# Kernel tuning notes

Hardware: AMD Instinct MI355X
Metric: run time of the kernel (lower is better)

The kernel has to match this reference:

```python
import jax, jax.numpy as jnp
import numpy as np

B, N, H, D, L = 2, 256, 256, 64, 6  # batch, pocket atoms, hidden dim, atom feat dim, EGNN layers


def _lin(x, w, b):
    return x @ w + b


def setup_inputs() -> dict:
    key = jax.random.key(0)
    ks = iter(jax.random.split(key, 64))

    def w(shape, s=0.05):
        return jax.random.normal(next(ks), shape, jnp.float32) * s

    inp = {
        'pocket_coords': jax.random.normal(next(ks), (B, N, 3), jnp.float32),
        'pocket_features': jax.random.normal(next(ks), (B, N, D), jnp.float32),
        't': jax.random.uniform(next(ks), (B,), jnp.float32, 0.0, 1000.0),
        'pe_w1': w((3 + D, H)), 'pe_b1': w((H,)),
        'pe_w2': w((H, H)), 'pe_b2': w((H,)),
        'pe_w3': w((H, H)), 'pe_b3': w((H,)),
        'te_w1': w((1, H)), 'te_b1': w((H,)),
        'te_w2': w((H, H)), 'te_b2': w((H,)),
        'ln_g': jnp.ones((L, H), jnp.float32), 'ln_b': jnp.zeros((L, H), jnp.float32),
        'ew1': w((L, 2 * H + 1, H)), 'eb1': w((L, H)),
        'ew2': w((L, H, H)), 'eb2': w((L, H)),
        'cw1': w((L, H, H)), 'cb1': w((L, H)),
        'cw2': w((L, H, 1)), 'cb2': w((L, 1)),
        'nw1': w((L, 2 * H, H)), 'nb1': w((L, H)),
        'nw2': w((L, H, H)), 'nb2': w((L, H)),
        'dec_w1': w((H, H)), 'dec_b1': w((H,)),
        'dec_w2': w((H, H)), 'dec_b2': w((H,)),
        'dec_w3': w((H, 3)), 'dec_b3': w((3,)),
    }
    return inp


def reference(pocket_coords, pocket_features, t,
              pe_w1, pe_b1, pe_w2, pe_b2, pe_w3, pe_b3,
              te_w1, te_b1, te_w2, te_b2,
              ln_g, ln_b,
              ew1, eb1, ew2, eb2,
              cw1, cb1, cw2, cb2,
              nw1, nb1, nw2, nb2,
              dec_w1, dec_b1, dec_w2, dec_b2, dec_w3, dec_b3):
    relu, silu = jax.nn.relu, jax.nn.silu

    # --- pocket encoder (residual MLP; in_dim 67 != H so no skip; dropout = identity at eval)
    pin = jnp.concatenate([pocket_coords, pocket_features], axis=-1)  # [B,N,3+D]
    h = relu(_lin(pin, pe_w1, pe_b1))
    h = relu(_lin(h, pe_w2, pe_b2))
    h = relu(_lin(h, pe_w3, pe_b3))

    # --- time embedding, broadcast over atoms
    te = relu(_lin(t[:, None], te_w1, te_b1))
    te = _lin(te, te_w2, te_b2)  # [B,H]
    h = h + te[:, None, :]

    # --- 6-layer dense EGNN (all-pairs), norm_feats=True -> LayerNorm on h per layer
    x = pocket_coords
    for l in range(L):
        h_in = h
        mu = h.mean(-1, keepdims=True)
        hc = h - mu
        hn = hc / jnp.sqrt((hc * hc).mean(-1, keepdims=True) + 1e-5) * ln_g[l] + ln_b[l]
        rel = x[:, :, None, :] - x[:, None, :, :]            # [B,N,N,3]
        d2 = jnp.sum(rel * rel, axis=-1, keepdims=True)      # [B,N,N,1]
        hi = jnp.broadcast_to(hn[:, :, None, :], (B, N, N, H))
        hj = jnp.broadcast_to(hn[:, None, :, :], (B, N, N, H))
        eij = jnp.concatenate([hi, hj, d2], axis=-1)         # [B,N,N,2H+1]
        m = silu(_lin(eij, ew1[l], eb1[l]))
        m = silu(_lin(m, ew2[l], eb2[l]))                    # [B,N,N,H] messages
        cw = _lin(silu(_lin(m, cw1[l], cb1[l])), cw2[l], cb2[l])  # [B,N,N,1]
        x = x + jnp.mean(rel * cw, axis=2)                   # equivariant coord update
        magg = jnp.sum(m, axis=2)                            # [B,N,H] aggregated messages
        u = silu(_lin(jnp.concatenate([hn, magg], axis=-1), nw1[l], nb1[l]))
        h = h_in + _lin(u, nw2[l], nb2[l])                   # residual node update

    # --- decoder (residual MLP, dims equal so skip applies before final projection)
    o = relu(_lin(h, dec_w1, dec_b1))
    o = relu(_lin(o, dec_w2, dec_b2)) + h
    return _lin(o, dec_w3, dec_b3)                           # predicted noise [B,N,3]
```

## Files before the change

### kernel.cpp

```cpp
#include <hip/hip_runtime.h>
#include <math.h>

static constexpr int NB = 2, NN = 256, HH = 256, DD = 64, LL = 6;
static constexpr int RN = NB * NN * HH;
static constexpr int SROWB = 528;

typedef __attribute__((ext_vector_type(8))) short bf16x8;
typedef __attribute__((ext_vector_type(4))) float f32x4;
typedef __attribute__((ext_vector_type(4))) float float4v;
typedef __attribute__((ext_vector_type(4))) unsigned int u32x4;

__device__ __forceinline__ float fsilu(float v) {
    return v * __builtin_amdgcn_rcpf(1.0f + __expf(-v));
}
__device__ __forceinline__ unsigned short f2bf(float f) {
    union { float f; unsigned int u; } x; x.f = f;
    unsigned int r = x.u + 0x7fffu + ((x.u >> 16) & 1u);
    return (unsigned short)(r >> 16);
}
__device__ __forceinline__ float bitsf(unsigned int u) {
    union { float f; unsigned int u; } x; x.u = u; return x.f;
}
__device__ __forceinline__ float bflo(unsigned int w) { return bitsf(w << 16); }
__device__ __forceinline__ float bfhi(unsigned int w) { return bitsf(w & 0xffff0000u); }
__device__ __forceinline__ unsigned int cvtpk(float lo, float hi) {
    unsigned int w;
    asm("v_cvt_pk_bf16_f32 %0, %1, %2" : "=v"(w) : "v"(lo), "v"(hi));
    return w;
}

__global__ void k_convert(const float* __restrict__ ew2, const float* __restrict__ cw1,
                          unsigned short* __restrict__ ew2P, unsigned short* __restrict__ cw1P) {
    int g = blockIdx.x * blockDim.x + threadIdx.x;
    if (g >= LL * 8192) return;
    int l = g >> 13;
    int r = g & 8191;
    int lane = r & 63;
    int fidx = r >> 6;
    int ks = fidx >> 4;
    int wv = (fidx >> 1) & 7;
    int ct = fidx & 1;
    int col = wv * 32 + ct * 16 + (lane & 15);
    int k0 = ks * 32 + (lane >> 4) * 8;
    #pragma unroll
    for (int e = 0; e < 8; ++e) {
        ew2P[(size_t)g * 8 + e] = f2bf(ew2[((size_t)l * HH + k0 + e) * HH + col]);
        cw1P[(size_t)g * 8 + e] = f2bf(cw1[((size_t)l * HH + k0 + e) * HH + col]);
    }
}

__global__ void k_convert2(const float* __restrict__ nw1, const float* __restrict__ nw2,
                           const float* __restrict__ ew1,
                           unsigned short* __restrict__ nw1B, unsigned short* __restrict__ nw2B,
                           unsigned short* __restrict__ ew1B) {
    int idx = blockIdx.x * blockDim.x + threadIdx.x;
    if (idx >= LL * 131072) return;
    int l = idx >> 17;
    int r = idx & 131071;
    int c = r >> 8, col = r & 255;
    int dst = (l << 17) + ((c >> 1) << 9) + (col << 1) + (c & 1);
    nw1B[dst] = f2bf(nw1[(size_t)l * 131072 + c * 256 + col]);
    ew1B[dst] = f2bf(ew1[(size_t)l * 131328 + c * 256 + col]);
    if (r < 65536) {
        int d2 = (l << 16) + ((c >> 1) << 9) + (col << 1) + (c & 1);
        nw2B[d2] = f2bf(nw2[(size_t)l * 65536 + c * 256 + col]);
    }
}

__global__ __launch_bounds__(256) void k_encoder(
    const float* __restrict__ coords, const float* __restrict__ feats, const float* __restrict__ t,
    const float* __restrict__ pw1, const float* __restrict__ pb1,
    const float* __restrict__ pw2, const float* __restrict__ pb2,
    const float* __restrict__ pw3, const float* __restrict__ pb3,
    const float* __restrict__ tw1, const float* __restrict__ tb1,
    const float* __restrict__ tw2, const float* __restrict__ tb2,
    float* __restrict__ h, float* __restrict__ x) {
    __shared__ float spinT[68][2];
    __shared__ float shaT[HH][2];
    __shared__ float shbT[HH][2];
    __shared__ float ste1[HH];
    int tid = threadIdx.x;
    int base = blockIdx.x * 2;
    int b = base / NN;

    #pragma unroll
    for (int r = 0; r < 2; ++r) {
        int row = base + r;
        if (tid < 3) spinT[tid][r] = coords[row * 3 + tid];
        if (tid < DD) spinT[3 + tid][r] = feats[row * DD + tid];
    }
    float tv = t[b];
    ste1[tid] = fmaxf(tv * tw1[tid] + tb1[tid], 0.0f);
    if (tid < 6) {
        int r = tid / 3, c = tid % 3;
        x[(base + r) * 3 + c] = coords[(base + r) * 3 + c];
    }
    __syncthreads();

    float a0 = pb1[tid], a1 = a0;
    for (int c = 0; c < 67; ++c) {
        float w = pw1[c * HH + tid];
        float2 s = *(const float2*)&spinT[c][0];
        a0 += s.x * w; a1 += s.y * w;
    }
    shaT[tid][0] = fmaxf(a0, 0.f); shaT[tid][1] = fmaxf(a1, 0.f);
    __syncthreads();
    a0 = pb2[tid]; a1 = a0;
    for (int c = 0; c < HH; ++c) {
        float w = pw2[c * HH + tid];
        float2 s = *(const float2*)&shaT[c][0];
        a0 += s.x * w; a1 += s.y * w;
    }
    shbT[tid][0] = fmaxf(a0, 0.f); shbT[tid][1] = fmaxf(a1, 0.f);
    __syncthreads();
    a0 = pb3[tid]; a1 = a0;
    float te = tb2[tid];
    for (int c = 0; c < HH; ++c) {
        float w = pw3[c * HH + tid];
        float2 s = *(const float2*)&shbT[c][0];
        a0 += s.x * w; a1 += s.y * w;
        te += ste1[c] * tw2[c * HH + tid];
    }
    h[(base + 0) * HH + tid] = fmaxf(a0, 0.f) + te;
    h[(base + 1) * HH + tid] = fmaxf(a1, 0.f) + te;
}

__global__ __launch_bounds__(256) void k_ln_aiaj(
    const float* __restrict__ h, const float* __restrict__ g, const float* __restrict__ bta,
    const unsigned int* __restrict__ ew1w, const float* __restrict__ eb1l,
    float* __restrict__ hn, float* __restrict__ Ai, unsigned short* __restrict__ AjB) {
    __shared__ float shnT[HH][2];
    int tid = threadIdx.x, wv = tid >> 6, lane = tid & 63;
    int base = blockIdx.x * 2;

    if (wv < 2) {
        int row = base + wv;
        float v[4];
        #pragma unroll
        for (int q = 0; q < 4; ++q) v[q] = h[row * HH + lane + 64 * q];
        float s = v[0] + v[1] + v[2] + v[3];
        #pragma unroll
        for (int m = 1; m < 64; m <<= 1) s += __shfl_xor(s, m);
        float mu = s * (1.0f / HH);
        float var = 0.f;
        #pragma unroll
        for (int q = 0; q < 4; ++q) { v[q] -= mu; var += v[q] * v[q]; }
        #pragma unroll
        for (int m = 1; m < 64; m <<= 1) var += __shfl_xor(var, m);
        float rstd = rsqrtf(var * (1.0f / HH) + 1e-5f);
        #pragma unroll
        for (int q = 0; q < 4; ++q) {
            int k = lane + 64 * q;
            float hv = v[q] * rstd * g[k] + bta[k];
            shnT[k][wv] = hv;
            hn[row * HH + k] = hv;
        }
    }
    __syncthreads();

    float ai0 = eb1l[tid], ai1 = ai0;
    float aj0 = 0.f, aj1 = 0.f;
    for (int c2 = 0; c2 < 128; ++c2) {
        unsigned int wip = ew1w[c2 * 256 + tid];
        unsigned int wjp = ew1w[(128 + c2) * 256 + tid];
        float4 s = *(const float4*)&shnT[c2 * 2][0];
        ai0 += s.x * bflo(wip) + s.z * bfhi(wip);
        ai1 += s.y * bflo(wip) + s.w * bfhi(wip);
        aj0 += s.x * bflo(wjp) + s.z * bfhi(wjp);
        aj1 += s.y * bflo(wjp) + s.w * bfhi(wjp);
    }
    Ai[(base + 0) * HH + tid] = ai0; AjB[(base + 0) * HH + tid] = f2bf(aj0);
    Ai[(base + 1) * HH + tid] = ai1; AjB[(base + 1) * HH + tid] = f2bf(aj1);
}

__global__ __launch_bounds__(512, 1) void k_edge(
    const float* __restrict__ x, const float* __restrict__ Ai, const unsigned short* __restrict__ AjB,
    const float* __restrict__ wd, const float* __restrict__ eb2v,
    const unsigned short* __restrict__ ew2P, const unsigned short* __restrict__ cw1P,
    const float* __restrict__ cb1v, const float* __restrict__ cw2v, const float* __restrict__ cb2p,
    float* __restrict__ h, float* __restrict__ hn,
    float* __restrict__ xnext, float* __restrict__ Ainext, unsigned short* __restrict__ AjBnext,
    const unsigned int* __restrict__ nw1w, const float* __restrict__ nb1l,
    const unsigned int* __restrict__ nw2w, const float* __restrict__ nb2l,
    const float* __restrict__ gamv, const float* __restrict__ betv,
    const unsigned int* __restrict__ ew1wn, const float* __restrict__ eb1n,
    int has_ln) {
    __shared__ float srel[128][3];
    __shared__ float sd2[128];
    __shared__ float cwpart[8][128];
    __shared__ float smagg[256];
    __shared__ char s_tile[128 * SROWB];
    __shared__ char m_tile[128 * SROWB];

    int tid = threadIdx.x, wv = tid >> 6, lane = tid & 63;
    int g4 = lane >> 4, l15 = lane & 15;
    int colbase = wv * 32;
    int bi = blockIdx.x;
    int b = bi >> 8, i = bi & 255;
    int ni = b * NN + i;
    int bbase = b * NN;
    int bthr = ((wv << 7) + lane) << 3;

    int k0p = (tid & 31) << 3;
    float aiv[8], wdv[8];
    {
        float4v a0 = *(const float4v*)(Ai + (size_t)ni * HH + k0p);
        float4v a1 = *(const float4v*)(Ai + (size_t)ni * HH + k0p + 4);
        float4v w0 = *(const float4v*)(wd + k0p);
        float4v w1 = *(const float4v*)(wd + k0p + 4);
        #pragma unroll
        for (int e = 0; e < 4; ++e) { aiv[e] = a0[e]; aiv[4 + e] = a1[e]; wdv[e] = w0[e]; wdv[4 + e] = w1[e]; }
    }
    float eb2r[2], cb1r[2], cw2r[2];
    #pragma unroll
    for (int ct = 0; ct < 2; ++ct) {
        int col = colbase + ct * 16 + l15;
        eb2r[ct] = eb2v[col]; cb1r[ct] = cb1v[col]; cw2r[ct] = cw2v[col];
    }
    float xi0 = x[ni * 3 + 0], xi1 = x[ni * 3 + 1], xi2 = x[ni * 3 + 2];
    float cb2 = cb2p[0];

    bf16x8 Bew[8][2], Bcw[8][2];
    #pragma unroll
    for (int ks = 0; ks < 8; ++ks) {
        #pragma unroll
        for (int ct = 0; ct < 2; ++ct) {
            Bew[ks][ct] = *(const bf16x8*)(ew2P + (ks << 13) + (ct << 9) + bthr);
            Bcw[ks][ct] = *(const bf16x8*)(cw1P + (ks << 13) + (ct << 9) + bthr);
        }
    }

    char* p1w = s_tile + ((tid >> 5) * SROWB + k0p * 2);
    const char* aA = s_tile + (l15 * SROWB + g4 * 16);
    const char* aM = m_tile + (l15 * SROWB + g4 * 16);
    char* mwA = m_tile + ((g4 * 4) * SROWB + (colbase + l15) * 2);
    float mgv[2] = {0.f, 0.f};
    float xd0 = 0.f, xd1 = 0.f, xd2 = 0.f;

    #pragma unroll 1
    for (int jc = 0; jc < 2; ++jc) {
        int j0 = jc * 128;
        __syncthreads();
        if (tid < 128) {
            int j = bbase + j0 + tid;
            float rx = xi0 - x[j * 3 + 0];
            float ry = xi1 - x[j * 3 + 1];
            float rz = xi2 - x[j * 3 + 2];
            srel[tid][0] = rx; srel[tid][1] = ry; srel[tid][2] = rz;
            sd2[tid] = rx * rx + ry * ry + rz * rz;
        }
        __syncthreads();

        #pragma unroll
        for (int it = 0; it < 8; ++it) {
            int row = it * 16 + (tid >> 5);
            float d2v = sd2[row];
            u32x4 ajw = *(const u32x4*)(AjB + ((size_t)(bbase + j0 + row) * HH + k0p));
            unsigned int uw0, uw1, uw2, uw3;
            uw0 = cvtpk(fsilu(aiv[0] + bflo(ajw[0]) + d2v * wdv[0]), fsilu(aiv[1] + bfhi(ajw[0]) + d2v * wdv[1]));
            uw1 = cvtpk(fsilu(aiv[2] + bflo(ajw[1]) + d2v * wdv[2]), fsilu(aiv[3] + bfhi(ajw[1]) + d2v * wdv[3]));
            uw2 = cvtpk(fsilu(aiv[4] + bflo(ajw[2]) + d2v * wdv[4]), fsilu(aiv[5] + bfhi(ajw[2]) + d2v * wdv[5]));
            uw3 = cvtpk(fsilu(aiv[6] + bflo(ajw[3]) + d2v * wdv[6]), fsilu(aiv[7] + bfhi(ajw[3]) + d2v * wdv[7]));
            u32x4 sv = {uw0, uw1, uw2, uw3};
            *reinterpret_cast<u32x4*>(p1w + it * 16 * SROWB) = sv;
        }
        __syncthreads();

        #pragma unroll 1
        for (int rh = 0; rh < 4; ++rh) {
            f32x4 acc[2][2];
            acc[0][0] = (f32x4){0.f,0.f,0.f,0.f}; acc[0][1] = (f32x4){0.f,0.f,0.f,0.f};
            acc[1][0] = (f32x4){0.f,0.f,0.f,0.f}; acc[1][1] = (f32x4){0.f,0.f,0.f,0.f};
            const char* aBase = aA + rh * 32 * SROWB;
            #pragma unroll
            for (int ks = 0; ks < 8; ++ks) {
                bf16x8 a0 = *reinterpret_cast<const bf16x8*>(aBase + ks * 64);
                bf16x8 a1 = *reinterpret_cast<const bf16x8*>(aBase + 16 * SROWB + ks * 64);
                acc[0][0] = __builtin_amdgcn_mfma_f32_16x16x32_bf16(a0, Bew[ks][0], acc[0][0], 0, 0, 0);
                acc[0][1] = __builtin_amdgcn_mfma_f32_16x16x32_bf16(a0, Bew[ks][1], acc[0][1], 0, 0, 0);
                acc[1][0] = __builtin_amdgcn_mfma_f32_16x16x32_bf16(a1, Bew[ks][0], acc[1][0], 0, 0, 0);
                acc[1][1] = __builtin_amdgcn_mfma_f32_16x16x32_bf16(a1, Bew[ks][1], acc[1][1], 0, 0, 0);
            }
            char* mw = mwA + rh * 32 * SROWB;
            #pragma unroll
            for (int rt = 0; rt < 2; ++rt) {
                #pragma unroll
                for (int r = 0; r < 4; ++r) {
                    float v0 = fsilu(acc[rt][0][r] + eb2r[0]);
                    float v1 = fsilu(acc[rt][1][r] + eb2r[1]);
                    mgv[0] += v0; mgv[1] += v1;
                    unsigned int w = cvtpk(v0, v1);
                    char* p = mw + (rt * 16 + r) * SROWB;
                    *reinterpret_cast<unsigned short*>(p) = (unsigned short)w;
                    *reinterpret_cast<unsigned short*>(p + 32) = (unsigned short)(w >> 16);
                }
            }
        }
        __syncthreads();

        #pragma unroll 1
        for (int rh = 0; rh < 4; ++rh) {
            f32x4 acc[2][2];
            acc[0][0] = (f32x4){0.f,0.f,0.f,0.f}; acc[0][1] = (f32x4){0.f,0.f,0.f,0.f};
            acc[1][0] = (f32x4){0.f,0.f,0.f,0.f}; acc[1][1] = (f32x4){0.f,0.f,0.f,0.f};
            const char* aBase = aM + rh * 32 * SROWB;
            #pragma unroll
            for (int ks = 0; ks < 8; ++ks) {
                bf16x8 a0 = *reinterpret_cast<const bf16x8*>(aBase + ks * 64);
                bf16x8 a1 = *reinterpret_cast<const bf16x8*>(aBase + 16 * SROWB + ks * 64);
                acc[0][0] = __builtin_amdgcn_mfma_f32_16x16x32_bf16(a0, Bcw[ks][0], acc[0][0], 0, 0, 0);
                acc[0][1] = __builtin_amdgcn_mfma_f32_16x16x32_bf16(a0, Bcw[ks][1], acc[0][1], 0, 0, 0);
                acc[1][0] = __builtin_amdgcn_mfma_f32_16x16x32_bf16(a1, Bcw[ks][0], acc[1][0], 0, 0, 0);
                acc[1][1] = __builtin_amdgcn_mfma_f32_16x16x32_bf16(a1, Bcw[ks][1], acc[1][1], 0, 0, 0);
            }
            float rs[8];
            #pragma unroll
            for (int q = 0; q < 8; ++q) rs[q] = 0.f;
            #pragma unroll
            for (int ct = 0; ct < 2; ++ct) {
                #pragma unroll
                for (int rt = 0; rt < 2; ++rt)
                    #pragma unroll
                    for (int r = 0; r < 4; ++r)
                        rs[rt * 4 + r] += fsilu(acc[rt][ct][r] + cb1r[ct]) * cw2r[ct];
            }
            #pragma unroll
            for (int m = 1; m <= 8; m <<= 1)
                #pragma unroll
                for (int q = 0; q < 8; ++q) rs[q] += __shfl_xor(rs[q], m);
            if (l15 == 0) {
                #pragma unroll
                for (int rt = 0; rt < 2; ++rt)
                    #pragma unroll
                    for (int r = 0; r < 4; ++r)
                        cwpart[wv][rh * 32 + rt * 16 + g4 * 4 + r] = rs[rt * 4 + r];
            }
        }
        __syncthreads();
        if (tid < 64) {
            #pragma unroll 1
            for (int q = 0; q < 2; ++q) {
                int lr = q * 64 + tid;
                float cwv = cb2;
                #pragma unroll
                for (int w = 0; w < 8; ++w) cwv += cwpart[w][lr];
                float p0 = srel[lr][0] * cwv;
                float p1 = srel[lr][1] * cwv;
                float p2 = srel[lr][2] * cwv;
                #pragma unroll
                for (int m = 1; m < 64; m <<= 1) {
                    p0 += __shfl_xor(p0, m); p1 += __shfl_xor(p1, m); p2 += __shfl_xor(p2, m);
                }
                xd0 += p0; xd1 += p1; xd2 += p2;
            }
        }
    }

    #pragma unroll
    for (int ct = 0; ct < 2; ++ct) {
        mgv[ct] += __shfl_xor(mgv[ct], 16);
        mgv[ct] += __shfl_xor(mgv[ct], 32);
    }
    if (lane < 16) {
        smagg[colbase + lane] = mgv[0];
        smagg[colbase + 16 + lane] = mgv[1];
    }
    if (has_ln && tid == 0) {
        xnext[ni * 3 + 0] = xi0 + xd0 * (1.0f / NN);
        xnext[ni * 3 + 1] = xi1 + xd1 * (1.0f / NN);
        xnext[ni * 3 + 2] = xi2 + xd2 * (1.0f / NN);
    }
    __syncthreads();

    float* s2v   = (float*)s_tile;
    float* part  = (float*)(s_tile + 4096);
    float* suv   = (float*)(s_tile + 8192);
    float* shrow = (float*)(s_tile + 12288);
    float* shnv  = (float*)(s_tile + 16384);
    float* red   = (float*)(s_tile + 20480);

    if (tid < 256) {
        s2v[tid] = hn[(size_t)ni * HH + tid];
        s2v[HH + tid] = smagg[tid];
    }
    __syncthreads();
    {
        int col = tid & 255, kh = tid >> 8;
        const unsigned int* w = nw1w + (kh * 128) * 256;
        const float* sv = s2v + kh * 256;
        float p = 0.f;
        for (int c2 = 0; c2 < 128; ++c2) {
            unsigned int wp = w[c2 * 256 + col];
            float2 sp = *(const float2*)&sv[c2 * 2];
            p += sp.x * bflo(wp) + sp.y * bfhi(wp);
        }
        part[tid] = p;
    }
    __syncthreads();
    if (tid < 256) suv[tid] = fsilu(part[tid] + part[256 + tid] + nb1l[tid]);
    __syncthreads();
    {
        int col = tid & 255, kh = tid >> 8;
        const unsigned int* w = nw2w + (kh * 64) * 256;
        const float* sv = suv + kh * 128;
        float p = 0.f;
        for (int c2 = 0; c2 < 64; ++c2) {
            unsigned int wp = w[c2 * 256 + col];
            float2 sp = *(const float2*)&sv[c2 * 2];
            p += sp.x * bflo(wp) + sp.y * bfhi(wp);
        }
        part[tid] = p;
    }
    __syncthreads();
    if (tid < 256) {
        float hv = h[(size_t)ni * HH + tid] + part[tid] + part[256 + tid] + nb2l[tid];
        h[(size_t)ni * HH + tid] = hv;
        shrow[tid] = hv;
    }
    __syncthreads();
    if (!has_ln) return;

    {
        float v = (tid < 256) ? shrow[tid] : 0.f;
        float s1 = v, sq = v * v;
        #pragma unroll
        for (int m = 1; m < 64; m <<= 1) { s1 += __shfl_xor(s1, m); sq += __shfl_xor(sq, m); }
        if (lane == 0) { red[wv] = s1; red[8 + wv] = sq; }
    }
    __syncthreads();
    {
        float mu  = (red[0] + red[1] + red[2] + red[3]) * (1.0f / HH);
        float msq = (red[8] + red[9] + red[10] + red[11]) * (1.0f / HH);
        float rstd = rsqrtf(msq - mu * mu + 1e-5f);
        if (tid < 256) {
            float hv = (shrow[tid] - mu) * rstd * gamv[tid] + betv[tid];
            shnv[tid] = hv;
            hn[(size_t)ni * HH + tid] = hv;
        }
    }
    __syncthreads();
    {
        int col = tid & 255, hf = tid >> 8;
        const unsigned int* w = ew1wn + (hf * 128) * 256;
        float p = (hf == 0) ? eb1n[col] : 0.f;
        for (int c2 = 0; c2 < 128; ++c2) {
            unsigned int wp = w[c2 * 256 + col];
            float2 sp = *(const float2*)&shnv[c2 * 2];
            p += sp.x * bflo(wp) + sp.y * bfhi(wp);
        }
        if (hf == 0) Ainext[(size_t)ni * HH + col] = p;
        else AjBnext[(size_t)ni * HH + col] = f2bf(p);
    }
}

__global__ __launch_bounds__(256) void k_decoder(
    const float* __restrict__ h,
    const float* __restrict__ dw1, const float* __restrict__ db1,
    const float* __restrict__ dw2, const float* __restrict__ db2,
    const float* __restrict__ dw3, const float* __restrict__ db3,
    float* __restrict__ out) {
    __shared__ float shT[HH][2];
    __shared__ float so1T[HH][2];
    __shared__ float so2T[HH][2];
    int tid = threadIdx.x;
    int base = blockIdx.x * 2;
    #pragma unroll
    for (int r = 0; r < 2; ++r) shT[tid][r] = h[(base + r) * HH + tid];
    __syncthreads();
    float a0 = db1[tid], a1 = a0;
    for (int c = 0; c < HH; ++c) {
        float w = dw1[c * HH + tid];
        float2 s = *(const float2*)&shT[c][0];
        a0 += s.x * w; a1 += s.y * w;
    }
    so1T[tid][0] = fmaxf(a0, 0.f); so1T[tid][1] = fmaxf(a1, 0.f);
    __syncthreads();
    a0 = db2[tid]; a1 = a0;
    for (int c = 0; c < HH; ++c) {
        float w = dw2[c * HH + tid];
        float2 s = *(const float2*)&so1T[c][0];
        a0 += s.x * w; a1 += s.y * w;
    }
    so2T[tid][0] = fmaxf(a0, 0.f) + shT[tid][0];
    so2T[tid][1] = fmaxf(a1, 0.f) + shT[tid][1];
    __syncthreads();
    if (tid < 6) {
        int r = tid / 3, c = tid % 3;
        float acc = db3[c];
        for (int k = 0; k < HH; ++k) acc += so2T[k][r] * dw3[k * 3 + c];
        out[(base + r) * 3 + c] = acc;
    }
}

extern "C" void kernel_launch(void* const* d_in, const int* in_sizes, int n_in,
                              void* d_out, int out_size, void* d_ws, size_t ws_size,
                              hipStream_t stream) {
    const float* coords = (const float*)d_in[0];
    const float* feats  = (const float*)d_in[1];
    const float* t      = (const float*)d_in[2];
    const float* pe_w1  = (const float*)d_in[3];  const float* pe_b1 = (const float*)d_in[4];
    const float* pe_w2  = (const float*)d_in[5];  const float* pe_b2 = (const float*)d_in[6];
    const float* pe_w3  = (const float*)d_in[7];  const float* pe_b3 = (const float*)d_in[8];
    const float* te_w1  = (const float*)d_in[9];  const float* te_b1 = (const float*)d_in[10];
    const float* te_w2  = (const float*)d_in[11]; const float* te_b2 = (const float*)d_in[12];
    const float* ln_g   = (const float*)d_in[13]; const float* ln_b  = (const float*)d_in[14];
    const float* ew1    = (const float*)d_in[15]; const float* eb1   = (const float*)d_in[16];
    const float* ew2    = (const float*)d_in[17]; const float* eb2   = (const float*)d_in[18];
    const float* cw1    = (const float*)d_in[19]; const float* cb1   = (const float*)d_in[20];
    const float* cw2    = (const float*)d_in[21]; const float* cb2   = (const float*)d_in[22];
    const float* nw1    = (const float*)d_in[23]; const float* nb1   = (const float*)d_in[24];
    const float* nw2    = (const float*)d_in[25]; const float* nb2   = (const float*)d_in[26];
    const float* dec_w1 = (const float*)d_in[27]; const float* dec_b1 = (const float*)d_in[28];
    const float* dec_w2 = (const float*)d_in[29]; const float* dec_b2 = (const float*)d_in[30];
    const float* dec_w3 = (const float*)d_in[31]; const float* dec_b3 = (const float*)d_in[32];

    float* ws = (float*)d_ws;
    float* h    = ws;
    float* hn   = ws + RN;
    float* Ai0  = ws + 2 * RN;
    float* Ai1  = ws + 3 * RN;
    float* xb0  = ws + 4 * RN;
    float* xb1  = ws + 4 * RN + 2048;
    unsigned short* Aj0  = (unsigned short*)(ws + 4 * RN + 4096);
    unsigned short* Aj1  = Aj0 + RN;
    unsigned short* ew2P = Aj1 + RN;
    unsigned short* cw1P = ew2P + LL * HH * HH;
    unsigned short* nw1B = cw1P + LL * HH * HH;
    unsigned short* ew1B = nw1B + LL * 2 * HH * HH;
    unsigned short* nw2B = ew1B + LL * 2 * HH * HH;

    k_convert<<<(LL * 8192 + 511) / 512, 512, 0, stream>>>(ew2, cw1, ew2P, cw1P);
    k_convert2<<<(LL * 131072 + 255) / 256, 256, 0, stream>>>(nw1, nw2, ew1, nw1B, nw2B, ew1B);
    k_encoder<<<NB * NN / 2, 256, 0, stream>>>(coords, feats, t,
        pe_w1, pe_b1, pe_w2, pe_b2, pe_w3, pe_b3, te_w1, te_b1, te_w2, te_b2, h, xb0);
    k_ln_aiaj<<<NB * NN / 2, 256, 0, stream>>>(h, ln_g, ln_b,
        (const unsigned int*)ew1B, eb1, hn, Ai0, Aj0);

    for (int l = 0; l < LL; ++l) {
        const float* xin = (l & 1) ? xb1 : xb0;
        float* xout      = (l & 1) ? xb0 : xb1;
        const float* AiIn = (l & 1) ? Ai1 : Ai0;
        float* AiOut      = (l & 1) ? Ai0 : Ai1;
        const unsigned short* AjIn = (l & 1) ? Aj1 : Aj0;
        unsigned short* AjOut      = (l & 1) ? Aj0 : Aj1;
        int ln = (l + 1 < LL) ? (l + 1) : LL - 1;
        k_edge<<<NB * NN, 512, 0, stream>>>(xin, AiIn, AjIn,
            ew1 + ((size_t)l * 513 + 512) * HH, eb2 + l * HH,
            ew2P + (size_t)l * HH * HH, cw1P + (size_t)l * HH * HH,
            cb1 + l * HH, cw2 + l * HH, cb2 + l,
            h, hn, xout, AiOut, AjOut,
            (const unsigned int*)(nw1B + (size_t)l * 2 * HH * HH), nb1 + l * HH,
            (const unsigned int*)(nw2B + (size_t)l * HH * HH), nb2 + l * HH,
            ln_g + ln * HH, ln_b + ln * HH,
            (const unsigned int*)(ew1B + (size_t)ln * 2 * HH * HH), eb1 + ln * HH,
            (l + 1 < LL) ? 1 : 0);
    }

    k_decoder<<<NB * NN / 2, 256, 0, stream>>>(h, dec_w1, dec_b1, dec_w2, dec_b2,
                                               dec_w3, dec_b3, (float*)d_out);
}
```

Baseline: 580.9 us.

## Process two target atoms per edge block to amortize weight loads

Each k_edge block now handles two consecutive atoms i instead of one, so the grid shrinks from 512 to 256 blocks. The register-resident ew2/cw1 B fragments are loaded once and reused across both atoms. The node-update, LayerNorm and next-layer Ai/Aj matvecs now process both rows together, which halves weight reads per row. On the other hand, 256 blocks at one block per CU may leave some CUs idle on a 256-CU part, and the per-block serial work doubles.

After: 515.2 us. -11.3%, faster.

```diff
diff --git a/kernel.cpp b/kernel.cpp
--- a/kernel.cpp
+++ b/kernel.cpp
@@ -188,28 +188,26 @@
     __shared__ float srel[128][3];
     __shared__ float sd2[128];
     __shared__ float cwpart[8][128];
-    __shared__ float smagg[256];
-    __shared__ char s_tile[128 * SROWB];
-    __shared__ char m_tile[128 * SROWB];
+    __shared__ float smagg2[2][256];
+    __shared__ __attribute__((aligned(16))) char s_tile[128 * SROWB];
+    __shared__ __attribute__((aligned(16))) char m_tile[128 * SROWB];
 
     int tid = threadIdx.x, wv = tid >> 6, lane = tid & 63;
     int g4 = lane >> 4, l15 = lane & 15;
     int colbase = wv * 32;
-    int bi = blockIdx.x;
-    int b = bi >> 8, i = bi & 255;
-    int ni = b * NN + i;
+    int ni0 = blockIdx.x * 2;
+    int ni1 = ni0 + 1;
+    int b = ni0 >> 8;
     int bbase = b * NN;
     int bthr = ((wv << 7) + lane) << 3;
-
     int k0p = (tid & 31) << 3;
-    float aiv[8], wdv[8];
+
+    float wdv[8];
     {
-        float4v a0 = *(const float4v*)(Ai + (size_t)ni * HH + k0p);
-        float4v a1 = *(const float4v*)(Ai + (size_t)ni * HH + k0p + 4);
         float4v w0 = *(const float4v*)(wd + k0p);
         float4v w1 = *(const float4v*)(wd + k0p + 4);
         #pragma unroll
-        for (int e = 0; e < 4; ++e) { aiv[e] = a0[e]; aiv[4 + e] = a1[e]; wdv[e] = w0[e]; wdv[4 + e] = w1[e]; }
+        for (int e = 0; e < 4; ++e) { wdv[e] = w0[e]; wdv[4 + e] = w1[e]; }
     }
     float eb2r[2], cb1r[2], cw2r[2];
     #pragma unroll
@@ -217,7 +215,6 @@
         int col = colbase + ct * 16 + l15;
         eb2r[ct] = eb2v[col]; cb1r[ct] = cb1v[col]; cw2r[ct] = cw2v[col];
     }
-    float xi0 = x[ni * 3 + 0], xi1 = x[ni * 3 + 1], xi2 = x[ni * 3 + 2];
     float cb2 = cb2p[0];
 
     bf16x8 Bew[8][2], Bcw[8][2];
@@ -234,222 +231,258 @@
     const char* aA = s_tile + (l15 * SROWB + g4 * 16);
     const char* aM = m_tile + (l15 * SROWB + g4 * 16);
     char* mwA = m_tile + ((g4 * 4) * SROWB + (colbase + l15) * 2);
-    float mgv[2] = {0.f, 0.f};
-    float xd0 = 0.f, xd1 = 0.f, xd2 = 0.f;
 
     #pragma unroll 1
-    for (int jc = 0; jc < 2; ++jc) {
-        int j0 = jc * 128;
-        __syncthreads();
-        if (tid < 128) {
-            int j = bbase + j0 + tid;
-            float rx = xi0 - x[j * 3 + 0];
-            float ry = xi1 - x[j * 3 + 1];
-            float rz = xi2 - x[j * 3 + 2];
-            srel[tid][0] = rx; srel[tid][1] = ry; srel[tid][2] = rz;
-            sd2[tid] = rx * rx + ry * ry + rz * rz;
-        }
-        __syncthreads();
-
-        #pragma unroll
-        for (int it = 0; it < 8; ++it) {
-            int row = it * 16 + (tid >> 5);
-            float d2v = sd2[row];
-            u32x4 ajw = *(const u32x4*)(AjB + ((size_t)(bbase + j0 + row) * HH + k0p));
-            unsigned int uw0, uw1, uw2, uw3;
-            uw0 = cvtpk(fsilu(aiv[0] + bflo(ajw[0]) + d2v * wdv[0]), fsilu(aiv[1] + bfhi(ajw[0]) + d2v * wdv[1]));
-            uw1 = cvtpk(fsilu(aiv[2] + bflo(ajw[1]) + d2v * wdv[2]), fsilu(aiv[3] + bfhi(ajw[1]) + d2v * wdv[3]));
-            uw2 = cvtpk(fsilu(aiv[4] + bflo(ajw[2]) + d2v * wdv[4]), fsilu(aiv[5] + bfhi(ajw[2]) + d2v * wdv[5]));
-            uw3 = cvtpk(fsilu(aiv[6] + bflo(ajw[3]) + d2v * wdv[6]), fsilu(aiv[7] + bfhi(ajw[3]) + d2v * wdv[7]));
-            u32x4 sv = {uw0, uw1, uw2, uw3};
-            *reinterpret_cast<u32x4*>(p1w + it * 16 * SROWB) = sv;
-        }
-        __syncthreads();
+    for (int ir = 0; ir < 2; ++ir) {
+        int ni = ni0 + ir;
+        float aiv[8];
+        {
+            float4v a0 = *(const float4v*)(Ai + (size_t)ni * HH + k0p);
+            float4v a1 = *(const float4v*)(Ai + (size_t)ni * HH + k0p + 4);
+            #pragma unroll
+            for (int e = 0; e < 4; ++e) { aiv[e] = a0[e]; aiv[4 + e] = a1[e]; }
+        }
+        float xi0 = x[ni * 3 + 0], xi1 = x[ni * 3 + 1], xi2 = x[ni * 3 + 2];
+        float mgv[2] = {0.f, 0.f};
+        float xd0 = 0.f, xd1 = 0.f, xd2 = 0.f;
 
         #pragma unroll 1
-        for (int rh = 0; rh < 4; ++rh) {
-            f32x4 acc[2][2];
-            acc[0][0] = (f32x4){0.f,0.f,0.f,0.f}; acc[0][1] = (f32x4){0.f,0.f,0.f,0.f};
-            acc[1][0] = (f32x4){0.f,0.f,0.f,0.f}; acc[1][1] = (f32x4){0.f,0.f,0.f,0.f};
-            const char* aBase = aA + rh * 32 * SROWB;
+        for (int jc = 0; jc < 2; ++jc) {
+            int j0 = jc * 128;
+            __syncthreads();
+            if (tid < 128) {
+                int j = bbase + j0 + tid;
+                float rx = xi0 - x[j * 3 + 0];
+                float ry = xi1 - x[j * 3 + 1];
+                float rz = xi2 - x[j * 3 + 2];
+                srel[tid][0] = rx; srel[tid][1] = ry; srel[tid][2] = rz;
+                sd2[tid] = rx * rx + ry * ry + rz * rz;
+            }
+            __syncthreads();
+
             #pragma unroll
-            for (int ks = 0; ks < 8; ++ks) {
-                bf16x8 a0 = *reinterpret_cast<const bf16x8*>(aBase + ks * 64);
-                bf16x8 a1 = *reinterpret_cast<const bf16x8*>(aBase + 16 * SROWB + ks * 64);
-                acc[0][0] = __builtin_amdgcn_mfma_f32_16x16x32_bf16(a0, Bew[ks][0], acc[0][0], 0, 0, 0);
-                acc[0][1] = __builtin_amdgcn_mfma_f32_16x16x32_bf16(a0, Bew[ks][1], acc[0][1], 0, 0, 0);
-                acc[1][0] = __builtin_amdgcn_mfma_f32_16x16x32_bf16(a1, Bew[ks][0], acc[1][0], 0, 0, 0);
-                acc[1][1] = __builtin_amdgcn_mfma_f32_16x16x32_bf16(a1, Bew[ks][1], acc[1][1], 0, 0, 0);
+            for (int it = 0; it < 8; ++it) {
+                int row = it * 16 + (tid >> 5);
+                float d2v = sd2[row];
+                u32x4 ajw = *(const u32x4*)(AjB + ((size_t)(bbase + j0 + row) * HH + k0p));
+                unsigned int uw0, uw1, uw2, uw3;
+                uw0 = cvtpk(fsilu(aiv[0] + bflo(ajw[0]) + d2v * wdv[0]), fsilu(aiv[1] + bfhi(ajw[0]) + d2v * wdv[1]));
+                uw1 = cvtpk(fsilu(aiv[2] + bflo(ajw[1]) + d2v * wdv[2]), fsilu(aiv[3] + bfhi(ajw[1]) + d2v * wdv[3]));
+                uw2 = cvtpk(fsilu(aiv[4] + bflo(ajw[2]) + d2v * wdv[4]), fsilu(aiv[5] + bfhi(ajw[2]) + d2v * wdv[5]));
+                uw3 = cvtpk(fsilu(aiv[6] + bflo(ajw[3]) + d2v * wdv[6]), fsilu(aiv[7] + bfhi(ajw[3]) + d2v * wdv[7]));
+                u32x4 sv = {uw0, uw1, uw2, uw3};
+                *reinterpret_cast<u32x4*>(p1w + it * 16 * SROWB) = sv;
             }
-            char* mw = mwA + rh * 32 * SROWB;
-            #pragma unroll
-            for (int rt = 0; rt < 2; ++rt) {
+            __syncthreads();
+
+            #pragma unroll 1
+            for (int rh = 0; rh < 4; ++rh) {
+                f32x4 acc[2][2];
+                acc[0][0] = (f32x4){0.f,0.f,0.f,0.f}; acc[0][1] = (f32x4){0.f,0.f,0.f,0.f};
+                acc[1][0] = (f32x4){0.f,0.f,0.f,0.f}; acc[1][1] = (f32x4){0.f,0.f,0.f,0.f};
+                const char* aBase = aA + rh * 32 * SROWB;
                 #pragma unroll
-                for (int r = 0; r < 4; ++r) {
-                    float v0 = fsilu(acc[rt][0][r] + eb2r[0]);
-                    float v1 = fsilu(acc[rt][1][r] + eb2r[1]);
-                    mgv[0] += v0; mgv[1] += v1;
-                    unsigned int w = cvtpk(v0, v1);
-                    char* p = mw + (rt * 16 + r) * SROWB;
-                    *reinterpret_cast<unsigned short*>(p) = (unsigned short)w;
-                    *reinterpret_cast<unsigned short*>(p + 32) = (unsigned short)(w >> 16);
+                for (int ks = 0; ks < 8; ++ks) {
+                    bf16x8 a0 = *reinterpret_cast<const bf16x8*>(aBase + ks * 64);
+                    bf16x8 a1 = *reinterpret_cast<const bf16x8*>(aBase + 16 * SROWB + ks * 64);
+                    acc[0][0] = __builtin_amdgcn_mfma_f32_16x16x32_bf16(a0, Bew[ks][0], acc[0][0], 0, 0, 0);
+                    acc[0][1] = __builtin_amdgcn_mfma_f32_16x16x32_bf16(a0, Bew[ks][1], acc[0][1], 0, 0, 0);
+                    acc[1][0] = __builtin_amdgcn_mfma_f32_16x16x32_bf16(a1, Bew[ks][0], acc[1][0], 0, 0, 0);
+                    acc[1][1] = __builtin_amdgcn_mfma_f32_16x16x32_bf16(a1, Bew[ks][1], acc[1][1], 0, 0, 0);
+                }
+                char* mw = mwA + rh * 32 * SROWB;
+                #pragma unroll
+                for (int rt = 0; rt < 2; ++rt) {
+                    #pragma unroll
+                    for (int r = 0; r < 4; ++r) {
+                        float v0 = fsilu(acc[rt][0][r] + eb2r[0]);
+                        float v1 = fsilu(acc[rt][1][r] + eb2r[1]);
+                        mgv[0] += v0; mgv[1] += v1;
+                        unsigned int w = cvtpk(v0, v1);
+                        char* p = mw + (rt * 16 + r) * SROWB;
+                        *reinterpret_cast<unsigned short*>(p) = (unsigned short)w;
+                        *reinterpret_cast<unsigned short*>(p + 32) = (unsigned short)(w >> 16);
+                    }
                 }
             }
-        }
-        __syncthreads();
-
-        #pragma unroll 1
-        for (int rh = 0; rh < 4; ++rh) {
-            f32x4 acc[2][2];
-            acc[0][0] = (f32x4){0.f,0.f,0.f,0.f}; acc[0][1] = (f32x4){0.f,0.f,0.f,0.f};
-            acc[1][0] = (f32x4){0.f,0.f,0.f,0.f}; acc[1][1] = (f32x4){0.f,0.f,0.f,0.f};
-            const char* aBase = aM + rh * 32 * SROWB;
-            #pragma unroll
-            for (int ks = 0; ks < 8; ++ks) {
-                bf16x8 a0 = *reinterpret_cast<const bf16x8*>(aBase + ks * 64);
-                bf16x8 a1 = *reinterpret_cast<const bf16x8*>(aBase + 16 * SROWB + ks * 64);
-                acc[0][0] = __builtin_amdgcn_mfma_f32_16x16x32_bf16(a0, Bcw[ks][0], acc[0][0], 0, 0, 0);
-                acc[0][1] = __builtin_amdgcn_mfma_f32_16x16x32_bf16(a0, Bcw[ks][1], acc[0][1], 0, 0, 0);
-                acc[1][0] = __builtin_amdgcn_mfma_f32_16x16x32_bf16(a1, Bcw[ks][0], acc[1][0], 0, 0, 0);
-                acc[1][1] = __builtin_amdgcn_mfma_f32_16x16x32_bf16(a1, Bcw[ks][1], acc[1][1], 0, 0, 0);
+            __syncthreads();
+
+            #pragma unroll 1
+            for (int rh = 0; rh < 4; ++rh) {
+                f32x4 acc[2][2];
+                acc[0][0] = (f32x4){0.f,0.f,0.f,0.f}; acc[0][1] = (f32x4){0.f,0.f,0.f,0.f};
+                acc[1][0] = (f32x4){0.f,0.f,0.f,0.f}; acc[1][1] = (f32x4){0.f,0.f,0.f,0.f};
+                const char* aBase = aM + rh * 32 * SROWB;
+                #pragma unroll
+                for (int ks = 0; ks < 8; ++ks) {
+                    bf16x8 a0 = *reinterpret_cast<const bf16x8*>(aBase + ks * 64);
+                    bf16x8 a1 = *reinterpret_cast<const bf16x8*>(aBase + 16 * SROWB + ks * 64);
+                    acc[0][0] = __builtin_amdgcn_mfma_f32_16x16x32_bf16(a0, Bcw[ks][0], acc[0][0], 0, 0, 0);
+                    acc[0][1] = __builtin_amdgcn_mfma_f32_16x16x32_bf16(a0, Bcw[ks][1], acc[0][1], 0, 0, 0);
+                    acc[1][0] = __builtin_amdgcn_mfma_f32_16x16x32_bf16(a1, Bcw[ks][0], acc[1][0], 0, 0, 0);
+                    acc[1][1] = __builtin_amdgcn_mfma_f32_16x16x32_bf16(a1, Bcw[ks][1], acc[1][1], 0, 0, 0);
+                }
+                float rs[8];
+                #pragma unroll
+                for (int q = 0; q < 8; ++q) rs[q] = 0.f;
+                #pragma unroll
+                for (int ct = 0; ct < 2; ++ct) {
+                    #pragma unroll
+                    for (int rt = 0; rt < 2; ++rt)
+                        #pragma unroll
+                        for (int r = 0; r < 4; ++r)
+                            rs[rt * 4 + r] += fsilu(acc[rt][ct][r] + cb1r[ct]) * cw2r[ct];
+                }
+                #pragma unroll
+                for (int m = 1; m <= 8; m <<= 1)
+                    #pragma unroll
+                    for (int q = 0; q < 8; ++q) rs[q] += __shfl_xor(rs[q], m);
+                if (l15 == 0) {
+                    #pragma unroll
+                    for (int rt = 0; rt < 2; ++rt)
+                        #pragma unroll
+                        for (int r = 0; r < 4; ++r)
+                            cwpart[wv][rh * 32 + rt * 16 + g4 * 4 + r] = rs[rt * 4 + r];
+                }
             }
-            float rs[8];
-            #pragma unroll
-            for (int q = 0; q < 8; ++q) rs[q] = 0.f;
-            #pragma unroll
-            for (int ct = 0; ct < 2; ++ct) {
-                #pragma unroll
-                for (int rt = 0; rt < 2; ++rt)
+            __syncthreads();
+            if (tid < 64) {
+                #pragma unroll 1
+                for (int q = 0; q < 2; ++q) {
+                    int lr = q * 64 + tid;
+                    float cwv = cb2;
                     #pragma unroll
-                    for (int r = 0; r < 4; ++r)
-                        rs[rt * 4 + r] += fsilu(acc[rt][ct][r] + cb1r[ct]) * cw2r[ct];
+                    for (int w = 0; w < 8; ++w) cwv += cwpart[w][lr];
+                    float p0 = srel[lr][0] * cwv;
+                    float p1 = srel[lr][1] * cwv;
+                    float p2 = srel[lr][2] * cwv;
+                    #pragma unroll
+                    for (int m = 1; m < 64; m <<= 1) {
+                        p0 += __shfl_xor(p0, m); p1 += __shfl_xor(p1, m); p2 += __shfl_xor(p2, m);
+                    }
+                    xd0 += p0; xd1 += p1; xd2 += p2;
+                }
             }
-            #pragma unroll
-            for (int m = 1; m <= 8; m <<= 1)
-                #pragma unroll
-                for (int q = 0; q < 8; ++q) rs[q] += __shfl_xor(rs[q], m);
-            if (l15 == 0) {
-                #pragma unroll
-                for (int rt = 0; rt < 2; ++rt)
-                    #pragma unroll
-                    for (int r = 0; r < 4; ++r)
-                        cwpart[wv][rh * 32 + rt * 16 + g4 * 4 + r] = rs[rt * 4 + r];
-            }
-        }
-        __syncthreads();
-        if (tid < 64) {
-            #pragma unroll 1
-            for (int q = 0; q < 2; ++q) {
-                int lr = q * 64 + tid;
-                float cwv = cb2;
-                #pragma unroll
-                for (int w = 0; w < 8; ++w) cwv += cwpart[w][lr];
-                float p0 = srel[lr][0] * cwv;
-                float p1 = srel[lr][1] * cwv;
-                float p2 = srel[lr][2] * cwv;
-                #pragma unroll
-                for (int m = 1; m < 64; m <<= 1) {
-                    p0 += __shfl_xor(p0, m); p1 += __shfl_xor(p1, m); p2 += __shfl_xor(p2, m);
-                }
-                xd0 += p0; xd1 += p1; xd2 += p2;
-            }
-        }
-    }
-
-    #pragma unroll
-    for (int ct = 0; ct < 2; ++ct) {
-        mgv[ct] += __shfl_xor(mgv[ct], 16);
-        mgv[ct] += __shfl_xor(mgv[ct], 32);
-    }
-    if (lane < 16) {
-        smagg[colbase + lane] = mgv[0];
-        smagg[colbase + 16 + lane] = mgv[1];
-    }
-    if (has_ln && tid == 0) {
-        xnext[ni * 3 + 0] = xi0 + xd0 * (1.0f / NN);
-        xnext[ni * 3 + 1] = xi1 + xd1 * (1.0f / NN);
-        xnext[ni * 3 + 2] = xi2 + xd2 * (1.0f / NN);
-    }
-    __syncthreads();
-
-    float* s2v   = (float*)s_tile;
-    float* part  = (float*)(s_tile + 4096);
-    float* suv   = (float*)(s_tile + 8192);
-    float* shrow = (float*)(s_tile + 12288);
-    float* shnv  = (float*)(s_tile + 16384);
-    float* red   = (float*)(s_tile + 20480);
+        }
+
+        #pragma unroll
+        for (int ct = 0; ct < 2; ++ct) {
+            mgv[ct] += __shfl_xor(mgv[ct], 16);
+            mgv[ct] += __shfl_xor(mgv[ct], 32);
+        }
+        if (lane < 16) {
+            smagg2[ir][colbase + lane] = mgv[0];
+            smagg2[ir][colbase + 16 + lane] = mgv[1];
+        }
+        if (has_ln && tid == 0) {
+            xnext[ni * 3 + 0] = xi0 + xd0 * (1.0f / NN);
+            xnext[ni * 3 + 1] = xi1 + xd1 * (1.0f / NN);
+            xnext[ni * 3 + 2] = xi2 + xd2 * (1.0f / NN);
+        }
+    }
+    __syncthreads();
+
+    float* s2T   = (float*)s_tile;
+    float* part0 = (float*)(s_tile + 4096);
+    float* part1 = (float*)(s_tile + 6144);
+    float* suT   = (float*)(s_tile + 8192);
+    float* shrow = (float*)(s_tile + 10240);
+    float* shnT  = (float*)(s_tile + 12288);
 
     if (tid < 256) {
-        s2v[tid] = hn[(size_t)ni * HH + tid];
-        s2v[HH + tid] = smagg[tid];
+        s2T[tid * 2 + 0] = hn[(size_t)ni0 * HH + tid];
+        s2T[tid * 2 + 1] = hn[(size_t)ni1 * HH + tid];
+        s2T[(HH + tid) * 2 + 0] = smagg2[0][tid];
+        s2T[(HH + tid) * 2 + 1] = smagg2[1][tid];
     }
     __syncthreads();
     {
         int col = tid & 255, kh = tid >> 8;
         const unsigned int* w = nw1w + (kh * 128) * 256;
-        const float* sv = s2v + kh * 256;
-        float p = 0.f;
+        const float* sv = s2T + kh * 512;
+        float p0 = 0.f, p1 = 0.f;
         for (int c2 = 0; c2 < 128; ++c2) {
             unsigned int wp = w[c2 * 256 + col];
-            float2 sp = *(const float2*)&sv[c2 * 2];
-            p += sp.x * bflo(wp) + sp.y * bfhi(wp);
-        }
-        part[tid] = p;
-    }
-    __syncthreads();
-    if (tid < 256) suv[tid] = fsilu(part[tid] + part[256 + tid] + nb1l[tid]);
+            float4 sp = *(const float4*)&sv[c2 * 4];
+            p0 += sp.x * bflo(wp) + sp.z * bfhi(wp);
+            p1 += sp.y * bflo(wp) + sp.w * bfhi(wp);
+        }
+        part0[tid] = p0; part1[tid] = p1;
+    }
+    __syncthreads();
+    if (tid < 256) {
+        float bb = nb1l[tid];
+        suT[tid * 2 + 0] = fsilu(part0[tid] + part0[256 + tid] + bb);
+        suT[tid * 2 + 1] = fsilu(part1[tid] + part1[256 + tid] + bb);
+    }
     __syncthreads();
     {
         int col = tid & 255, kh = tid >> 8;
         const unsigned int* w = nw2w + (kh * 64) * 256;
-        const float* sv = suv + kh * 128;
-        float p = 0.f;
+        const float* sv = suT + kh * 256;
+        float p0 = 0.f, p1 = 0.f;
         for (int c2 = 0; c2 < 64; ++c2) {
             unsigned int wp = w[c2 * 256 + col];
-            float2 sp = *(const float2*)&sv[c2 * 2];
-            p += sp.x * bflo(wp) + sp.y * bfhi(wp);
-        }
-        part[tid] = p;
+            float4 sp = *(const float4*)&sv[c2 * 4];
+            p0 += sp.x * bflo(wp) + sp.z * bfhi(wp);
+            p1 += sp.y * bflo(wp) + sp.w * bfhi(wp);
+        }
+        part0[tid] = p0; part1[tid] = p1;
     }
     __syncthreads();
     if (tid < 256) {
-        float hv = h[(size_t)ni * HH + tid] + part[tid] + part[256 + tid] + nb2l[tid];
-        h[(size_t)ni * HH + tid] = hv;
-        shrow[tid] = hv;
+        float bb = nb2l[tid];
+        float h0v = h[(size_t)ni0 * HH + tid] + part0[tid] + part0[256 + tid] + bb;
+        float h1v = h[(size_t)ni1 * HH + tid] + part1[tid] + part1[256 + tid] + bb;
+        h[(size_t)ni0 * HH + tid] = h0v;
+        h[(size_t)ni1 * HH + tid] = h1v;
+        shrow[tid * 2 + 0] = h0v;
+        shrow[tid * 2 + 1] = h1v;
     }
     __syncthreads();
     if (!has_ln) return;
 
-    {
-        float v = (tid < 256) ? shrow[tid] : 0.f;
-        float s1 = v, sq = v * v;
-        #pragma unroll
-        for (int m = 1; m < 64; m <<= 1) { s1 += __shfl_xor(s1, m); sq += __shfl_xor(sq, m); }
-        if (lane == 0) { red[wv] = s1; red[8 + wv] = sq; }
-    }
-    __syncthreads();
-    {
-        float mu  = (red[0] + red[1] + red[2] + red[3]) * (1.0f / HH);
-        float msq = (red[8] + red[9] + red[10] + red[11]) * (1.0f / HH);
-        float rstd = rsqrtf(msq - mu * mu + 1e-5f);
-        if (tid < 256) {
-            float hv = (shrow[tid] - mu) * rstd * gamv[tid] + betv[tid];
-            shnv[tid] = hv;
-            hn[(size_t)ni * HH + tid] = hv;
+    if (wv < 2) {
+        float v[4];
+        #pragma unroll
+        for (int q = 0; q < 4; ++q) v[q] = shrow[(lane + 64 * q) * 2 + wv];
+        float s = v[0] + v[1] + v[2] + v[3];
+        #pragma unroll
+        for (int m = 1; m < 64; m <<= 1) s += __shfl_xor(s, m);
+        float mu = s * (1.0f / HH);
+        float var = 0.f;
+        #pragma unroll
+        for (int q = 0; q < 4; ++q) { v[q] -= mu; var += v[q] * v[q]; }
+        #pragma unroll
+        for (int m = 1; m < 64; m <<= 1) var += __shfl_xor(var, m);
+        float rstd = rsqrtf(var * (1.0f / HH) + 1e-5f);
+        #pragma unroll
+        for (int q = 0; q < 4; ++q) {
+            int k = lane + 64 * q;
+            float hv = v[q] * rstd * gamv[k] + betv[k];
+            shnT[k * 2 + wv] = hv;
+            hn[(size_t)(ni0 + wv) * HH + k] = hv;
         }
     }
     __syncthreads();
     {
         int col = tid & 255, hf = tid >> 8;
         const unsigned int* w = ew1wn + (hf * 128) * 256;
-        float p = (hf == 0) ? eb1n[col] : 0.f;
+        float p0 = (hf == 0) ? eb1n[col] : 0.f;
+        float p1 = p0;
         for (int c2 = 0; c2 < 128; ++c2) {
             unsigned int wp = w[c2 * 256 + col];
-            float2 sp = *(const float2*)&shnv[c2 * 2];
-            p += sp.x * bflo(wp) + sp.y * bfhi(wp);
-        }
-        if (hf == 0) Ainext[(size_t)ni * HH + col] = p;
-        else AjBnext[(size_t)ni * HH + col] = f2bf(p);
+            float4 sp = *(const float4*)&shnT[c2 * 4];
+            p0 += sp.x * bflo(wp) + sp.z * bfhi(wp);
+            p1 += sp.y * bflo(wp) + sp.w * bfhi(wp);
+        }
+        if (hf == 0) {
+            Ainext[(size_t)ni0 * HH + col] = p0;
+            Ainext[(size_t)ni1 * HH + col] = p1;
+        } else {
+            AjBnext[(size_t)ni0 * HH + col] = f2bf(p0);
+            AjBnext[(size_t)ni1 * HH + col] = f2bf(p1);
+        }
     }
 }
 
@@ -544,7 +577,7 @@
         const unsigned short* AjIn = (l & 1) ? Aj1 : Aj0;
         unsigned short* AjOut      = (l & 1) ? Aj0 : Aj1;
         int ln = (l + 1 < LL) ? (l + 1) : LL - 1;
-        k_edge<<<NB * NN, 512, 0, stream>>>(xin, AiIn, AjIn,
+        k_edge<<<NB * NN / 2, 512, 0, stream>>>(xin, AiIn, AjIn,
             ew1 + ((size_t)l * 513 + 512) * HH, eb2 + l * HH,
             ew2P + (size_t)l * HH * HH, cw1P + (size_t)l * HH * HH,
             cb1 + l * HH, cw2 + l * HH, cb2 + l,
```
